# Optimization experiments

Hardware: AMD Instinct MI355X
Metric: run time of the kernel (lower is better)

The kernel has to match this reference:

```python
import jax, jax.numpy as jnp
import numpy as np

V_THRESH = 0.3

@jax.custom_vjp
def spike(x):
    return (x > 0).astype(x.dtype)

def _spike_fwd(x):
    return spike(x), x

def _spike_bwd(x, g):
    # rectangular straight-through surrogate gradient (pass grad where |x| < 0.5)
    return (g * (jnp.abs(x) < 0.5).astype(g.dtype),)

spike.defvjp(_spike_fwd, _spike_bwd)


def setup_inputs() -> dict:
    key = jax.random.key(0)
    B, T, H = 128, 2048, 128
    k1, = jax.random.split(key, 1)
    x_seq = jax.random.normal(k1, (B, T, H), dtype=jnp.float32)
    v0 = jnp.zeros((B, H), dtype=jnp.float32)
    z0 = jnp.zeros((B, H), dtype=jnp.float32)
    decay_raw = jnp.zeros((H,), dtype=jnp.float32)  # nn.initializers.constant(0.0)
    return {"x_seq": x_seq, "v0": v0, "z0": z0, "decay_raw": decay_raw}


def reference(x_seq, v0, z0, decay_raw):
    # LIF recurrence: v_t = v_{t-1} * decay * (1 - z_{t-1}) + x_t ; z_t = spike(v_t - v_thresh)
    decay = jax.nn.sigmoid(decay_raw)  # (H,)

    def step(carry, x_t):
        v, z = carry
        v = v * decay * (1.0 - z) + x_t
        z_out = spike(v - V_THRESH)
        return (v, z_out), z_out

    x_tb = jnp.swapaxes(x_seq, 0, 1)  # [T, B, H] for lax.scan over time
    (_, _), spk_tb = jax.lax.scan(step, (v0, z0), x_tb)
    return jnp.swapaxes(spk_tb, 0, 1)  # [B, T, H]
```

## Files before the change

kernel.cpp:

```cpp
#include <hip/hip_runtime.h>
#include <math.h>


constexpr int Bdim = 128;
constexpr int Tdim = 2048;
constexpr int Hdim = 128;
constexpr int U = 32;
constexpr float VTH = 0.3f;

__global__ __launch_bounds__(64) void lif_kernel(
    const float* __restrict__ x,
    const float* __restrict__ v0,
    const float* __restrict__ z0,
    const float* __restrict__ decay_raw,
    float* __restrict__ out)
{
    const int tid = blockIdx.x * 64 + threadIdx.x;
    const int b = tid >> 7;
    const int h = tid & (Hdim - 1);

    const float decay = 1.0f / (1.0f + expf(-decay_raw[h]));
    float v = v0[tid];
    float z = z0[tid];

    const float* xp = x   + (size_t)b * Tdim * Hdim + h;
    float*       op = out + (size_t)b * Tdim * Hdim + h;

    float cur[U], nxt[U];

#pragma unroll
    for (int u = 0; u < U; ++u) cur[u] = xp[u * Hdim];

    for (int tc = 0; tc < Tdim; tc += U) {
        if (tc + U < Tdim) {
            const float* xn = xp + (size_t)(tc + U) * Hdim;
#pragma unroll
            for (int u = 0; u < U; ++u) nxt[u] = xn[u * Hdim];
        }
#pragma unroll
        for (int u = 0; u < U; ++u) {
            const float vd = v * decay;
            v = ((z > 0.5f) ? 0.0f : vd) + cur[u];
            z = (v > VTH) ? 1.0f : 0.0f;
            op[(size_t)(tc + u) * Hdim] = z;
        }
#pragma unroll
        for (int u = 0; u < U; ++u) cur[u] = nxt[u];
    }
}

extern "C" void kernel_launch(void* const* d_in, const int* in_sizes, int n_in,
                              void* d_out, int out_size, void* d_ws, size_t ws_size,
                              hipStream_t stream) {
    const float* x         = (const float*)d_in[0];
    const float* v0        = (const float*)d_in[1];
    const float* z0        = (const float*)d_in[2];
    const float* decay_raw = (const float*)d_in[3];
    float* out = (float*)d_out;

    const int total = Bdim * Hdim;
    lif_kernel<<<total / 64, 64, 0, stream>>>(x, v0, z0, decay_raw, out);
}
```

Baseline: 264.4 us.

## Stream input tiles into LDS via async global_load_lds with double buffering

Replaces the per-thread register prefetch of 32 timesteps with a double-buffered shared-memory pipeline. Each wave uses 16-byte global_load_lds DMA to fetch 128-timestep by 64-channel tiles, loading the next tile while the recurrence consumes the current one. The aim is more bytes in flight per wave and lower register pressure in this latency-bound scan, which has only one wave per batch/half-channel slice. The cost is 64KB of LDS per block and a barrier each tile, and correctness depends on the barrier also waiting for the async LDS loads to finish.

Result: faster. 248.0 us (-6.2%).

```diff
diff --git a/kernel.cpp b/kernel.cpp
--- a/kernel.cpp
+++ b/kernel.cpp
@@ -5,8 +5,12 @@
 constexpr int Bdim = 128;
 constexpr int Tdim = 2048;
 constexpr int Hdim = 128;
-constexpr int U = 32;
+constexpr int HW   = 64;
+constexpr int U    = 128;
 constexpr float VTH = 0.3f;
+
+typedef const __attribute__((address_space(1))) void* gptr_t;
+typedef __attribute__((address_space(3))) void* lptr_t;
 
 __global__ __launch_bounds__(64) void lif_kernel(
     const float* __restrict__ x,
@@ -15,37 +19,54 @@
     const float* __restrict__ decay_raw,
     float* __restrict__ out)
 {
-    const int tid = blockIdx.x * 64 + threadIdx.x;
-    const int b = tid >> 7;
-    const int h = tid & (Hdim - 1);
+    __shared__ float lds[2][U][HW];
+
+    const int lane = threadIdx.x;
+    const int w  = blockIdx.x;
+    const int b  = w >> 1;
+    const int h0 = (w & 1) * HW;
+    const int h  = h0 + lane;
 
     const float decay = 1.0f / (1.0f + expf(-decay_raw[h]));
-    float v = v0[tid];
-    float z = z0[tid];
+    float v = v0[b * Hdim + h];
+    float z = z0[b * Hdim + h];
 
-    const float* xp = x   + (size_t)b * Tdim * Hdim + h;
-    float*       op = out + (size_t)b * Tdim * Hdim + h;
+    const float* xbase = x   + (size_t)b * Tdim * Hdim + h0;
+    float*       obase = out + (size_t)b * Tdim * Hdim + h0 + lane;
 
-    float cur[U], nxt[U];
+    const int sub_r = lane >> 4;
+    const int sub_c = (lane & 15) * 4;
 
-#pragma unroll
-    for (int u = 0; u < U; ++u) cur[u] = xp[u * Hdim];
+    auto issue_tile = [&](int t0, int buf) {
+        const float* g = xbase + (size_t)t0 * Hdim + sub_c + (size_t)sub_r * Hdim;
+        #pragma unroll
+        for (int j = 0; j < U / 4; ++j) {
+            __builtin_amdgcn_global_load_lds(
+                (gptr_t)(const void*)(g + (size_t)(4 * j) * Hdim),
+                (lptr_t)(void*)&lds[buf][4 * j][0],
+                16, 0, 0);
+        }
+    };
 
+    issue_tile(0, 0);
+    __syncthreads();
+
+    int buf = 0;
     for (int tc = 0; tc < Tdim; tc += U) {
-        if (tc + U < Tdim) {
-            const float* xn = xp + (size_t)(tc + U) * Hdim;
-#pragma unroll
-            for (int u = 0; u < U; ++u) nxt[u] = xn[u * Hdim];
+        if (tc + U < Tdim) issue_tile(tc + U, buf ^ 1);
+
+        float* op = obase + (size_t)tc * Hdim;
+        #pragma unroll 16
+        for (int tl = 0; tl < U; ++tl) {
+            const float xv = lds[buf][tl][lane];
+            const float vd = v * decay;
+            v = ((z > 0.5f) ? 0.0f : vd) + xv;
+            z = (v > VTH) ? 1.0f : 0.0f;
+            op[(size_t)tl * Hdim] = z;
         }
-#pragma unroll
-        for (int u = 0; u < U; ++u) {
-            const float vd = v * decay;
-            v = ((z > 0.5f) ? 0.0f : vd) + cur[u];
-            z = (v > VTH) ? 1.0f : 0.0f;
-            op[(size_t)(tc + u) * Hdim] = z;
-        }
-#pragma unroll
-        for (int u = 0; u < U; ++u) cur[u] = nxt[u];
+
+        __syncthreads();
+        buf ^= 1;
     }
 }
 
@@ -58,6 +79,5 @@
     const float* decay_raw = (const float*)d_in[3];
     float* out = (float*)d_out;
 
-    const int total = Bdim * Hdim;
-    lif_kernel<<<total / 64, 64, 0, stream>>>(x, v0, z0, decay_raw, out);
+    lif_kernel<<<Bdim * Hdim / HW, 64, 0, stream>>>(x, v0, z0, decay_raw, out);
 }
```
